# Kernel tuning notes

Hardware: AMD Instinct MI355X
Metric: run time of the kernel (lower is better)

Reference implementation:

```python
import jax, jax.numpy as jnp
import numpy as np

N_NODES = 50000
N_EDGES = 800000


def setup_inputs() -> dict:
    key = jax.random.key(0)
    ks = jax.random.split(key, 8)
    x = jax.random.normal(ks[0], (N_NODES, 128), dtype=jnp.float32)
    edge_index = jax.random.randint(ks[1], (2, N_EDGES), 0, N_NODES, dtype=jnp.int64)
    # GCNConv weights (PyG: x @ W then propagate, bias after aggregation)
    W1 = jax.random.normal(ks[2], (128, 256), dtype=jnp.float32) / np.sqrt(128)
    b1 = jnp.zeros((256,), dtype=jnp.float32)
    W2 = jax.random.normal(ks[3], (256, 128), dtype=jnp.float32) / np.sqrt(256)
    b2 = jnp.zeros((128,), dtype=jnp.float32)
    # projection head
    fcW1 = jax.random.normal(ks[4], (128, 128), dtype=jnp.float32) / np.sqrt(128)
    fcb1 = jnp.zeros((128,), dtype=jnp.float32)
    fcW2 = jax.random.normal(ks[5], (128, 128), dtype=jnp.float32) / np.sqrt(128)
    fcb2 = jnp.zeros((128,), dtype=jnp.float32)
    return {"x": x, "edge_index": edge_index, "W1": W1, "b1": b1,
            "W2": W2, "b2": b2, "fcW1": fcW1, "fcb1": fcb1,
            "fcW2": fcW2, "fcb2": fcb2}


def _gcn_conv(x, W, b, src, dst, dinv):
    # x' = D^-1/2 (A + I) D^-1/2 (x W) + b  (GCN with self-loops)
    xw = x @ W                                             # [N, C]
    coeff = dinv[src] * dinv[dst]                          # [E]
    msg = xw[src] * coeff[:, None]                         # [E, C] gather
    agg = jax.ops.segment_sum(msg, dst, num_segments=N_NODES)  # scatter-add
    self_term = xw * (dinv * dinv)[:, None]                # self-loop
    return agg + self_term + b


def reference(x, edge_index, W1, b1, W2, b2, fcW1, fcb1, fcW2, fcb2):
    src, dst = edge_index[0], edge_index[1]
    # degree of A + I (in-degree on dst, weight 1 each, +1 self-loop)
    deg = jax.ops.segment_sum(jnp.ones((N_EDGES,), jnp.float32), dst,
                              num_segments=N_NODES) + 1.0
    dinv = jax.lax.rsqrt(deg)
    # Encoder: GCNConv -> relu -> GCNConv -> relu
    h = jax.nn.relu(_gcn_conv(x, W1, b1, src, dst, dinv))
    z = jax.nn.relu(_gcn_conv(h, W2, b2, src, dst, dinv))
    # projection: Linear -> ELU -> Linear
    p = jax.nn.elu(z @ fcW1 + fcb1)
    return p @ fcW2 + fcb2
```

## Files before the change

### kernel.cpp

```cpp
#include <hip/hip_runtime.h>
#include <hip/hip_bf16.h>
#include <cstdint>

#define N_NODES 50000
#define N_EDGES 800000
#define C128 128
#define SCAN_BLOCKS ((N_NODES + 255) / 256)

typedef __attribute__((ext_vector_type(8))) short bf16x8;
typedef __attribute__((ext_vector_type(4))) float f32x4;
typedef unsigned int u32;

__device__ __forceinline__ bf16x8 pack_bf16x8(u32 a, u32 b, u32 c, u32 d) {
    union { u32 u[4]; bf16x8 v; } x;
    x.u[0] = a; x.u[1] = b; x.u[2] = c; x.u[3] = d;
    return x.v;
}

__device__ __forceinline__ bf16x8 as_bf16x8(uint4 v) {
    union { uint4 u; bf16x8 b; } x;
    x.u = v;
    return x.b;
}

__device__ __forceinline__ u32 rne_bf16(float x) {
    u32 u = __float_as_uint(x);
    return (u + 0x7FFFu + ((u >> 16) & 1u)) >> 16;
}

__device__ __forceinline__ void stage16(const u32* g, u32* lds) {
    __builtin_amdgcn_global_load_lds(
        (const __attribute__((address_space(1))) u32*)g,
        (__attribute__((address_space(3))) u32*)lds, 16, 0, 0);
}


__global__ void k_zero(int* __restrict__ a, int* __restrict__ b, int n) {
    int i = blockIdx.x * blockDim.x + threadIdx.x;
    if (i < n) { a[i] = 0; b[i] = 0; }
}

__device__ __forceinline__ int clamp_node(int v) {
    return v < 0 ? 0 : (v >= N_NODES ? N_NODES - 1 : v);
}

__global__ void k_count(const int* __restrict__ ei, int* __restrict__ counts) {
    int e = blockIdx.x * blockDim.x + threadIdx.x;
    if (e < N_EDGES) {
        int dst = clamp_node(ei[N_EDGES + e]);
        atomicAdd(&counts[dst], 1);
    }
}

__global__ void k_dinv(const int* __restrict__ counts, float* __restrict__ dinv) {
    int i = blockIdx.x * blockDim.x + threadIdx.x;
    if (i < N_NODES) {
        dinv[i] = rsqrtf((float)counts[i] + 1.0f);
    }
}

__global__ __launch_bounds__(256) void k_xscale(const float* __restrict__ x,
                                                const float* __restrict__ dinv,
                                                u32* __restrict__ xs ) {
    int idx = blockIdx.x * 256 + threadIdx.x;
    if (idx < N_NODES * 32) {
        int node = idx >> 5;
        float di = dinv[node];
        float4 v = reinterpret_cast<const float4*>(x)[idx];
        u32 w0 = rne_bf16(v.x * di) | (rne_bf16(v.y * di) << 16);
        u32 w1 = rne_bf16(v.z * di) | (rne_bf16(v.w * di) << 16);
        reinterpret_cast<uint2*>(xs)[idx] = make_uint2(w0, w1);
    }
}

__global__ __launch_bounds__(256) void k_scan1(const int* __restrict__ counts,
                                               int* __restrict__ part,
                                               int* __restrict__ bsum) {
    __shared__ int s[256];
    const int tid = threadIdx.x;
    const int i = blockIdx.x * 256 + tid;
    int v = (i < N_NODES) ? counts[i] : 0;
    s[tid] = v;
    __syncthreads();
    for (int off = 1; off < 256; off <<= 1) {
        int t = (tid >= off) ? s[tid - off] : 0;
        __syncthreads();
        s[tid] += t;
        __syncthreads();
    }
    if (i < N_NODES) part[i] = s[tid];
    if (tid == 255) bsum[blockIdx.x] = s[255];
}

__global__ __launch_bounds__(256) void k_scan2(const int* __restrict__ bsum,
                                               int* __restrict__ boff) {
    __shared__ int s[256];
    const int tid = threadIdx.x;
    int v = (tid < SCAN_BLOCKS) ? bsum[tid] : 0;
    s[tid] = v;
    __syncthreads();
    for (int off = 1; off < 256; off <<= 1) {
        int t = (tid >= off) ? s[tid - off] : 0;
        __syncthreads();
        s[tid] += t;
        __syncthreads();
    }
    if (tid < SCAN_BLOCKS) boff[tid] = s[tid] - v;
}

__global__ __launch_bounds__(256) void k_scan3(const int* __restrict__ part,
                                               const int* __restrict__ counts,
                                               const int* __restrict__ boff,
                                               int* __restrict__ offsets) {
    const int i = blockIdx.x * 256 + threadIdx.x;
    if (i < N_NODES) offsets[i] = part[i] - counts[i] + boff[blockIdx.x];
    if (i == 0) offsets[N_NODES] = N_EDGES;
}

__global__ void k_fill(const int* __restrict__ ei, const int* __restrict__ offsets,
                       int* __restrict__ cursor, int* __restrict__ csr) {
    int e = blockIdx.x * blockDim.x + threadIdx.x;
    if (e < N_EDGES) {
        int src = clamp_node(ei[e]);
        int dst = clamp_node(ei[N_EDGES + e]);
        int pos = atomicAdd(&cursor[dst], 1);
        int slot = offsets[dst] + pos;
        if (slot < N_EDGES) csr[slot] = src;
    }
}


__global__ __launch_bounds__(64) void k_prep(const float* __restrict__ W1,
                                             const float* __restrict__ W2,
                                             const float* __restrict__ fcW1,
                                             const float* __restrict__ fcW2,
                                             u32* __restrict__ ftab) {
    int bx = blockIdx.x;
    int s = bx >> 5, f = bx & 31;
    int kf = f >> 3, nf = f & 7;
    int l = threadIdx.x;
    const float* src; int ld, roff, coff;
    switch (s) {
        case 0:  src = W1;   ld = 256; roff = 0;   coff = 0;   break;
        case 1:  src = W1;   ld = 256; roff = 0;   coff = 128; break;
        case 2:  src = W2;   ld = 128; roff = 0;   coff = 0;   break;
        case 3:  src = W2;   ld = 128; roff = 128; coff = 0;   break;
        case 4:  src = fcW1; ld = 128; roff = 0;   coff = 0;   break;
        default: src = fcW2; ld = 128; roff = 0;   coff = 0;   break;
    }
    int col = coff + nf * 16 + (l & 15);
    int krow = roff + kf * 32 + (l >> 4) * 8;
    u32 hp[4], lp[4];
#pragma unroll
    for (int p = 0; p < 4; ++p) {
        float a0 = src[(size_t)(krow + 2 * p) * ld + col];
        float a1 = src[(size_t)(krow + 2 * p + 1) * ld + col];
        u32 h0 = __float_as_uint(a0) & 0xFFFF0000u;
        u32 h1 = __float_as_uint(a1) & 0xFFFF0000u;
        float r0 = a0 - __uint_as_float(h0);
        float r1 = a1 - __uint_as_float(h1);
        hp[p] = (h0 >> 16) | h1;
        lp[p] = ((__float_as_uint(r0) & 0xFFFF0000u) >> 16) |
                (__float_as_uint(r1) & 0xFFFF0000u);
    }
    u32* secb = ftab + (size_t)s * 16384;
    *reinterpret_cast<uint4*>(secb + (size_t)f * 256 + 4 * l)        = make_uint4(hp[0], hp[1], hp[2], hp[3]);
    *reinterpret_cast<uint4*>(secb + 8192 + (size_t)f * 256 + 4 * l) = make_uint4(lp[0], lp[1], lp[2], lp[3]);
}


template <bool HAS_BIAS, bool RELU>
__global__ __launch_bounds__(256) void k_prop(const u32* __restrict__ xs,
                                              float* __restrict__ out,
                                              const float* __restrict__ dinv,
                                              const int* __restrict__ offsets,
                                              const int* __restrict__ csr,
                                              const float* __restrict__ bias) {
    const int wave = threadIdx.x >> 6;
    const int lane = threadIdx.x & 63;
    const int half = lane >> 5;
    const int lc   = lane & 31;
    const int node = (blockIdx.x * 4 + wave) * 2 + half;
    if (node >= N_NODES) return;

    const uint2* __restrict__ xp = reinterpret_cast<const uint2*>(xs);
    const float di = dinv[node];

    uint2 sv = xp[(size_t)node * 32 + lc];
    float ax = __uint_as_float(sv.x << 16);
    float ay = __uint_as_float(sv.x & 0xFFFF0000u);
    float az = __uint_as_float(sv.y << 16);
    float aw = __uint_as_float(sv.y & 0xFFFF0000u);

    int e = offsets[node];
    const int eend = offsets[node + 1];
    for (; e + 4 <= eend; e += 4) {
        int s0 = csr[e + 0], s1 = csr[e + 1], s2 = csr[e + 2], s3 = csr[e + 3];
        uint2 v0 = xp[(size_t)s0 * 32 + lc];
        uint2 v1 = xp[(size_t)s1 * 32 + lc];
        uint2 v2 = xp[(size_t)s2 * 32 + lc];
        uint2 v3 = xp[(size_t)s3 * 32 + lc];
        ax += __uint_as_float(v0.x << 16);
        ay += __uint_as_float(v0.x & 0xFFFF0000u);
        az += __uint_as_float(v0.y << 16);
        aw += __uint_as_float(v0.y & 0xFFFF0000u);
        ax += __uint_as_float(v1.x << 16);
        ay += __uint_as_float(v1.x & 0xFFFF0000u);
        az += __uint_as_float(v1.y << 16);
        aw += __uint_as_float(v1.y & 0xFFFF0000u);
        ax += __uint_as_float(v2.x << 16);
        ay += __uint_as_float(v2.x & 0xFFFF0000u);
        az += __uint_as_float(v2.y << 16);
        aw += __uint_as_float(v2.y & 0xFFFF0000u);
        ax += __uint_as_float(v3.x << 16);
        ay += __uint_as_float(v3.x & 0xFFFF0000u);
        az += __uint_as_float(v3.y << 16);
        aw += __uint_as_float(v3.y & 0xFFFF0000u);
    }
    for (; e < eend; ++e) {
        int s = csr[e];
        uint2 v = xp[(size_t)s * 32 + lc];
        ax += __uint_as_float(v.x << 16);
        ay += __uint_as_float(v.x & 0xFFFF0000u);
        az += __uint_as_float(v.y << 16);
        aw += __uint_as_float(v.y & 0xFFFF0000u);
    }

    float4 o;
    o.x = di * ax; o.y = di * ay; o.z = di * az; o.w = di * aw;
    if (HAS_BIAS) {
        float4 bb = reinterpret_cast<const float4*>(bias)[lc];
        o.x += bb.x; o.y += bb.y; o.z += bb.z; o.w += bb.w;
    }
    if (RELU) {
        o.x = fmaxf(o.x, 0.0f); o.y = fmaxf(o.y, 0.0f);
        o.z = fmaxf(o.z, 0.0f); o.w = fmaxf(o.w, 0.0f);
    }
    reinterpret_cast<float4*>(out)[(size_t)node * 32 + lc] = o;
}


template <int NHALF, int ACT1, bool FINAL_BIAS, bool BF16_OUT>
__global__ __launch_bounds__(256, 3) void k_fused(
        const float* __restrict__ A,
        const u32* __restrict__ ftabW1,
        const u32* __restrict__ ftabW2,
        const float* __restrict__ b1v,
        const float* __restrict__ b2v,
        float* __restrict__ C,
        u32* __restrict__ C16,
        const float* __restrict__ dscale,
        int M) {
    __shared__ u32 lds_w[8192];

    const int tid = threadIdx.x;
    const int wave = tid >> 6, l = tid & 63;
    const int l15 = l & 15, l4 = l >> 4;
    const int r = blockIdx.x * 64 + wave * 16 + l15;
    const float* arow = A + (size_t)(r < M ? r : M - 1) * 128;

    auto stage_hi = [&](const u32* sec) {
#pragma unroll
        for (int i = 0; i < 8; ++i) {
            int off = i * 1024 + wave * 256;
            stage16(sec + off + 4 * l, lds_w + off);
        }
    };

    f32x4 accQ[8] = {};

    stage_hi(ftabW1);
    __syncthreads();

#pragma unroll
    for (int half = 0; half < NHALF; ++half) {
        const u32* w1lo = ftabW1 + (size_t)half * 16384 + 8192;
        const u32* w2lo = ftabW2 + (size_t)half * 16384 + 8192;

        f32x4 accH[8] = {};
#pragma unroll
        for (int kf = 0; kf < 4; ++kf) {
            uint4 wl[8];
#pragma unroll
            for (int nf = 0; nf < 8; ++nf)
                wl[nf] = *reinterpret_cast<const uint4*>(
                    w1lo + (size_t)(kf * 8 + nf) * 256 + 4 * l);

            const float* ap = arow + kf * 32 + l4 * 8;
            float4 v0 = *reinterpret_cast<const float4*>(ap);
            float4 v1 = *reinterpret_cast<const float4*>(ap + 4);
            float av[8] = {v0.x, v0.y, v0.z, v0.w, v1.x, v1.y, v1.z, v1.w};
            u32 hp[4], lp[4];
#pragma unroll
            for (int p = 0; p < 4; ++p) {
                float a0 = av[2 * p], a1 = av[2 * p + 1];
                u32 h0 = __float_as_uint(a0) & 0xFFFF0000u;
                u32 h1 = __float_as_uint(a1) & 0xFFFF0000u;
                float q0 = a0 - __uint_as_float(h0);
                float q1 = a1 - __uint_as_float(h1);
                hp[p] = (h0 >> 16) | h1;
                lp[p] = ((__float_as_uint(q0) & 0xFFFF0000u) >> 16) |
                        (__float_as_uint(q1) & 0xFFFF0000u);
            }
            bf16x8 ahi = pack_bf16x8(hp[0], hp[1], hp[2], hp[3]);
            bf16x8 alo = pack_bf16x8(lp[0], lp[1], lp[2], lp[3]);

#pragma unroll
            for (int nf = 0; nf < 8; ++nf) {
                bf16x8 whi = as_bf16x8(*reinterpret_cast<const uint4*>(
                    lds_w + (kf * 8 + nf) * 256 + 4 * l));
                bf16x8 wlo = as_bf16x8(wl[nf]);
                accH[nf] = __builtin_amdgcn_mfma_f32_16x16x32_bf16(whi, ahi, accH[nf], 0, 0, 0);
                accH[nf] = __builtin_amdgcn_mfma_f32_16x16x32_bf16(whi, alo, accH[nf], 0, 0, 0);
                accH[nf] = __builtin_amdgcn_mfma_f32_16x16x32_bf16(wlo, ahi, accH[nf], 0, 0, 0);
            }
        }
        __syncthreads();
        stage_hi(ftabW2 + (size_t)half * 16384);

        u32 hpk[8][4];
#pragma unroll
        for (int nf = 0; nf < 8; ++nf) {
            const float4 bb = *reinterpret_cast<const float4*>(
                b1v + half * 128 + nf * 16 + l4 * 4);
            const float bbv[4] = {bb.x, bb.y, bb.z, bb.w};
#pragma unroll
            for (int reg = 0; reg < 4; ++reg) {
                float v = accH[nf][reg] + bbv[reg];
                if (ACT1 == 1) v = fmaxf(v, 0.0f);
                else           v = v > 0.0f ? v : (expf(v) - 1.0f);
                u32 vh = __float_as_uint(v) & 0xFFFF0000u;
                float rr = v - __uint_as_float(vh);
                hpk[nf][reg] = (vh >> 16) | (__float_as_uint(rr) & 0xFFFF0000u);
            }
        }
        __syncthreads();

#pragma unroll
        for (int kf = 0; kf < 4; ++kf) {
            uint4 wl[8];
#pragma unroll
            for (int nf = 0; nf < 8; ++nf)
                wl[nf] = *reinterpret_cast<const uint4*>(
                    w2lo + (size_t)(kf * 8 + nf) * 256 + 4 * l);

            u32 got[8];
#pragma unroll
            for (int je = 0; je < 8; ++je) {
                int srcLane = ((l4 & 1) * 2 + (je >> 2)) * 16 + l15;
                u32 g0 = __shfl(hpk[2 * kf][je & 3], srcLane, 64);
                u32 g1 = __shfl(hpk[2 * kf + 1][je & 3], srcLane, 64);
                got[je] = (l4 & 2) ? g1 : g0;
            }
            u32 hh[4], gg[4];
#pragma unroll
            for (int p = 0; p < 4; ++p) {
                hh[p] = (got[2 * p] & 0xFFFFu) | (got[2 * p + 1] << 16);
                gg[p] = (got[2 * p] >> 16) | (got[2 * p + 1] & 0xFFFF0000u);
            }
            bf16x8 bh = pack_bf16x8(hh[0], hh[1], hh[2], hh[3]);
            bf16x8 bl = pack_bf16x8(gg[0], gg[1], gg[2], gg[3]);

#pragma unroll
            for (int nf = 0; nf < 8; ++nf) {
                bf16x8 whi = as_bf16x8(*reinterpret_cast<const uint4*>(
                    lds_w + (kf * 8 + nf) * 256 + 4 * l));
                bf16x8 wlo = as_bf16x8(wl[nf]);
                accQ[nf] = __builtin_amdgcn_mfma_f32_16x16x32_bf16(whi, bh, accQ[nf], 0, 0, 0);
                accQ[nf] = __builtin_amdgcn_mfma_f32_16x16x32_bf16(whi, bl, accQ[nf], 0, 0, 0);
                accQ[nf] = __builtin_amdgcn_mfma_f32_16x16x32_bf16(wlo, bh, accQ[nf], 0, 0, 0);
            }
        }

        if (half + 1 < NHALF) {
            __syncthreads();
            stage_hi(ftabW1 + (size_t)(half + 1) * 16384);
            __syncthreads();
        }
    }

    if (r < M) {
        if (BF16_OUT) {
            float sc = dscale[r];
#pragma unroll
            for (int nf = 0; nf < 8; ++nf) {
                u32 w0 = rne_bf16(accQ[nf][0] * sc) | (rne_bf16(accQ[nf][1] * sc) << 16);
                u32 w1 = rne_bf16(accQ[nf][2] * sc) | (rne_bf16(accQ[nf][3] * sc) << 16);
                reinterpret_cast<uint2*>(C16)[(size_t)r * 32 + nf * 4 + l4] =
                    make_uint2(w0, w1);
            }
        } else {
#pragma unroll
            for (int nf = 0; nf < 8; ++nf) {
                float4 v;
                v.x = accQ[nf][0]; v.y = accQ[nf][1];
                v.z = accQ[nf][2]; v.w = accQ[nf][3];
                if (FINAL_BIAS) {
                    const float4 bb = *reinterpret_cast<const float4*>(b2v + nf * 16 + l4 * 4);
                    v.x += bb.x; v.y += bb.y; v.z += bb.z; v.w += bb.w;
                }
                *reinterpret_cast<float4*>(C + (size_t)r * 128 + nf * 16 + l4 * 4) = v;
            }
        }
    }
}


extern "C" void kernel_launch(void* const* d_in, const int* in_sizes, int n_in,
                              void* d_out, int out_size, void* d_ws, size_t ws_size,
                              hipStream_t stream) {
    const float* x    = (const float*)d_in[0];
    const int*   ei   = (const int*)d_in[1];
    const float* W1   = (const float*)d_in[2];
    const float* b1   = (const float*)d_in[3];
    const float* W2   = (const float*)d_in[4];
    const float* b2   = (const float*)d_in[5];
    const float* fcW1 = (const float*)d_in[6];
    const float* fcb1 = (const float*)d_in[7];
    const float* fcW2 = (const float*)d_in[8];
    const float* fcb2 = (const float*)d_in[9];
    float* out        = (float*)d_out;

    char* ws = (char*)d_ws;
    size_t off = 0;
    auto alloc = [&](size_t bytes) {
        void* p = ws + off;
        off += (bytes + 255) & ~(size_t)255;
        return p;
    };
    int*   counts  = (int*)alloc(N_NODES * sizeof(int));
    int*   cursor  = (int*)alloc(N_NODES * sizeof(int));
    int*   part    = (int*)alloc(N_NODES * sizeof(int));
    int*   bsum    = (int*)alloc(SCAN_BLOCKS * sizeof(int));
    int*   boff    = (int*)alloc(SCAN_BLOCKS * sizeof(int));
    int*   offsets = (int*)alloc((N_NODES + 1) * sizeof(int));
    int*   csr     = (int*)alloc(N_EDGES * sizeof(int));
    float* dinv    = (float*)alloc(N_NODES * sizeof(float));
    u32*   ftab    = (u32*)alloc((size_t)6 * 16384 * sizeof(u32));
    u32*   xs      = (u32*)alloc((size_t)N_NODES * 128 * 2);
    u32*   qs      = (u32*)alloc((size_t)N_NODES * 128 * 2);
    (void)ws_size; (void)n_in; (void)in_sizes; (void)out_size;

    const u32 SEC = 16384;

    k_zero<<<(N_NODES + 255) / 256, 256, 0, stream>>>(counts, cursor, N_NODES);
    k_prep<<<192, 64, 0, stream>>>(W1, W2, fcW1, fcW2, ftab);
    k_count<<<(N_EDGES + 255) / 256, 256, 0, stream>>>(ei, counts);
    k_dinv<<<(N_NODES + 255) / 256, 256, 0, stream>>>(counts, dinv);
    k_xscale<<<(N_NODES * 32 + 255) / 256, 256, 0, stream>>>(x, dinv, xs);
    k_scan1<<<SCAN_BLOCKS, 256, 0, stream>>>(counts, part, bsum);
    k_scan2<<<1, 256, 0, stream>>>(bsum, boff);
    k_scan3<<<SCAN_BLOCKS, 256, 0, stream>>>(part, counts, boff, offsets);
    k_fill<<<(N_EDGES + 255) / 256, 256, 0, stream>>>(ei, offsets, cursor, csr);

    const int prop_grid = (N_NODES + 7) / 8;
    const int gm = (N_NODES + 63) / 64;

    k_prop<false, false><<<prop_grid, 256, 0, stream>>>(xs, out, dinv, offsets, csr, nullptr);

    k_fused<2, 1, false, true><<<gm, 256, 0, stream>>>(out, ftab, ftab + 2 * SEC,
                                                       b1, nullptr, nullptr, qs, dinv, N_NODES);

    k_prop<true, true><<<prop_grid, 256, 0, stream>>>(qs, out, dinv, offsets, csr, b2);

    k_fused<1, 2, true, false><<<gm, 256, 0, stream>>>(out, ftab + 4 * SEC, ftab + 5 * SEC,
                                                       fcb1, fcb2, out, nullptr, nullptr, N_NODES);
}
```

Before: 238.6 us.

## Stage both hi and lo weight fragments in LDS and hoist A-row split

The weight fragment table is reorganised so each fragment's hi and lo bf16 halves sit next to each other (512-word stride). The fused MLP kernel now stages the whole section, hi and lo, into a doubled 64KB LDS buffer instead of reading the lo half from global memory per k-step. The input row's bf16 hi/lo split is also hoisted out of the half loop and computed once. In exchange the LDS use doubles and the occupancy hint drops from 3 to 2 blocks per CU, and the hoisted A fragments hold more registers.

```diff
diff --git a/kernel.cpp b/kernel.cpp
--- a/kernel.cpp
+++ b/kernel.cpp
@@ -163,9 +163,9 @@
         lp[p] = ((__float_as_uint(r0) & 0xFFFF0000u) >> 16) |
                 (__float_as_uint(r1) & 0xFFFF0000u);
     }
-    u32* secb = ftab + (size_t)s * 16384;
-    *reinterpret_cast<uint4*>(secb + (size_t)f * 256 + 4 * l)        = make_uint4(hp[0], hp[1], hp[2], hp[3]);
-    *reinterpret_cast<uint4*>(secb + 8192 + (size_t)f * 256 + 4 * l) = make_uint4(lp[0], lp[1], lp[2], lp[3]);
+    u32* dst = ftab + (size_t)s * 16384 + (size_t)f * 512;
+    *reinterpret_cast<uint4*>(dst + 4 * l)       = make_uint4(hp[0], hp[1], hp[2], hp[3]);
+    *reinterpret_cast<uint4*>(dst + 256 + 4 * l) = make_uint4(lp[0], lp[1], lp[2], lp[3]);
 }
 
 
@@ -241,7 +241,7 @@
 
 
 template <int NHALF, int ACT1, bool FINAL_BIAS, bool BF16_OUT>
-__global__ __launch_bounds__(256, 3) void k_fused(
+__global__ __launch_bounds__(256, 2) void k_fused(
         const float* __restrict__ A,
         const u32* __restrict__ ftabW1,
         const u32* __restrict__ ftabW2,
@@ -251,7 +251,7 @@
         u32* __restrict__ C16,
         const float* __restrict__ dscale,
         int M) {
-    __shared__ u32 lds_w[8192];
+    __shared__ u32 lds_w[16384];
 
     const int tid = threadIdx.x;
     const int wave = tid >> 6, l = tid & 63;
@@ -259,64 +259,58 @@
     const int r = blockIdx.x * 64 + wave * 16 + l15;
     const float* arow = A + (size_t)(r < M ? r : M - 1) * 128;
 
-    auto stage_hi = [&](const u32* sec) {
-#pragma unroll
-        for (int i = 0; i < 8; ++i) {
-            int off = i * 1024 + wave * 256;
+    auto stage_sec = [&](const u32* sec) {
+#pragma unroll
+        for (int i = 0; i < 16; ++i) {
+            int off = (i * 4 + wave) * 256;
             stage16(sec + off + 4 * l, lds_w + off);
         }
     };
 
+    bf16x8 ahi[4], alo[4];
+#pragma unroll
+    for (int kf = 0; kf < 4; ++kf) {
+        const float* ap = arow + kf * 32 + l4 * 8;
+        float4 v0 = *reinterpret_cast<const float4*>(ap);
+        float4 v1 = *reinterpret_cast<const float4*>(ap + 4);
+        float av[8] = {v0.x, v0.y, v0.z, v0.w, v1.x, v1.y, v1.z, v1.w};
+        u32 hp[4], lp[4];
+#pragma unroll
+        for (int p = 0; p < 4; ++p) {
+            float a0 = av[2 * p], a1 = av[2 * p + 1];
+            u32 h0 = __float_as_uint(a0) & 0xFFFF0000u;
+            u32 h1 = __float_as_uint(a1) & 0xFFFF0000u;
+            float q0 = a0 - __uint_as_float(h0);
+            float q1 = a1 - __uint_as_float(h1);
+            hp[p] = (h0 >> 16) | h1;
+            lp[p] = ((__float_as_uint(q0) & 0xFFFF0000u) >> 16) |
+                    (__float_as_uint(q1) & 0xFFFF0000u);
+        }
+        ahi[kf] = pack_bf16x8(hp[0], hp[1], hp[2], hp[3]);
+        alo[kf] = pack_bf16x8(lp[0], lp[1], lp[2], lp[3]);
+    }
+
     f32x4 accQ[8] = {};
 
-    stage_hi(ftabW1);
+    stage_sec(ftabW1);
     __syncthreads();
 
-#pragma unroll
     for (int half = 0; half < NHALF; ++half) {
-        const u32* w1lo = ftabW1 + (size_t)half * 16384 + 8192;
-        const u32* w2lo = ftabW2 + (size_t)half * 16384 + 8192;
-
         f32x4 accH[8] = {};
 #pragma unroll
         for (int kf = 0; kf < 4; ++kf) {
-            uint4 wl[8];
-#pragma unroll
-            for (int nf = 0; nf < 8; ++nf)
-                wl[nf] = *reinterpret_cast<const uint4*>(
-                    w1lo + (size_t)(kf * 8 + nf) * 256 + 4 * l);
-
-            const float* ap = arow + kf * 32 + l4 * 8;
-            float4 v0 = *reinterpret_cast<const float4*>(ap);
-            float4 v1 = *reinterpret_cast<const float4*>(ap + 4);
-            float av[8] = {v0.x, v0.y, v0.z, v0.w, v1.x, v1.y, v1.z, v1.w};
-            u32 hp[4], lp[4];
-#pragma unroll
-            for (int p = 0; p < 4; ++p) {
-                float a0 = av[2 * p], a1 = av[2 * p + 1];
-                u32 h0 = __float_as_uint(a0) & 0xFFFF0000u;
-                u32 h1 = __float_as_uint(a1) & 0xFFFF0000u;
-                float q0 = a0 - __uint_as_float(h0);
-                float q1 = a1 - __uint_as_float(h1);
-                hp[p] = (h0 >> 16) | h1;
-                lp[p] = ((__float_as_uint(q0) & 0xFFFF0000u) >> 16) |
-                        (__float_as_uint(q1) & 0xFFFF0000u);
-            }
-            bf16x8 ahi = pack_bf16x8(hp[0], hp[1], hp[2], hp[3]);
-            bf16x8 alo = pack_bf16x8(lp[0], lp[1], lp[2], lp[3]);
-
 #pragma unroll
             for (int nf = 0; nf < 8; ++nf) {
-                bf16x8 whi = as_bf16x8(*reinterpret_cast<const uint4*>(
-                    lds_w + (kf * 8 + nf) * 256 + 4 * l));
-                bf16x8 wlo = as_bf16x8(wl[nf]);
-                accH[nf] = __builtin_amdgcn_mfma_f32_16x16x32_bf16(whi, ahi, accH[nf], 0, 0, 0);
-                accH[nf] = __builtin_amdgcn_mfma_f32_16x16x32_bf16(whi, alo, accH[nf], 0, 0, 0);
-                accH[nf] = __builtin_amdgcn_mfma_f32_16x16x32_bf16(wlo, ahi, accH[nf], 0, 0, 0);
-            }
-        }
-        __syncthreads();
-        stage_hi(ftabW2 + (size_t)half * 16384);
+                const u32* fb = lds_w + (kf * 8 + nf) * 512;
+                bf16x8 whi = as_bf16x8(*reinterpret_cast<const uint4*>(fb + 4 * l));
+                bf16x8 wlo = as_bf16x8(*reinterpret_cast<const uint4*>(fb + 256 + 4 * l));
+                accH[nf] = __builtin_amdgcn_mfma_f32_16x16x32_bf16(whi, ahi[kf], accH[nf], 0, 0, 0);
+                accH[nf] = __builtin_amdgcn_mfma_f32_16x16x32_bf16(whi, alo[kf], accH[nf], 0, 0, 0);
+                accH[nf] = __builtin_amdgcn_mfma_f32_16x16x32_bf16(wlo, ahi[kf], accH[nf], 0, 0, 0);
+            }
+        }
+        __syncthreads();
+        stage_sec(ftabW2 + (size_t)half * 16384);
 
         u32 hpk[8][4];
 #pragma unroll
@@ -338,12 +332,6 @@
 
 #pragma unroll
         for (int kf = 0; kf < 4; ++kf) {
-            uint4 wl[8];
-#pragma unroll
-            for (int nf = 0; nf < 8; ++nf)
-                wl[nf] = *reinterpret_cast<const uint4*>(
-                    w2lo + (size_t)(kf * 8 + nf) * 256 + 4 * l);
-
             u32 got[8];
 #pragma unroll
             for (int je = 0; je < 8; ++je) {
@@ -363,9 +351,9 @@
 
 #pragma unroll
             for (int nf = 0; nf < 8; ++nf) {
-                bf16x8 whi = as_bf16x8(*reinterpret_cast<const uint4*>(
-                    lds_w + (kf * 8 + nf) * 256 + 4 * l));
-                bf16x8 wlo = as_bf16x8(wl[nf]);
+                const u32* fb = lds_w + (kf * 8 + nf) * 512;
+                bf16x8 whi = as_bf16x8(*reinterpret_cast<const uint4*>(fb + 4 * l));
+                bf16x8 wlo = as_bf16x8(*reinterpret_cast<const uint4*>(fb + 256 + 4 * l));
                 accQ[nf] = __builtin_amdgcn_mfma_f32_16x16x32_bf16(whi, bh, accQ[nf], 0, 0, 0);
                 accQ[nf] = __builtin_amdgcn_mfma_f32_16x16x32_bf16(whi, bl, accQ[nf], 0, 0, 0);
                 accQ[nf] = __builtin_amdgcn_mfma_f32_16x16x32_bf16(wlo, bh, accQ[nf], 0, 0, 0);
@@ -374,7 +362,7 @@
 
         if (half + 1 < NHALF) {
             __syncthreads();
-            stage_hi(ftabW1 + (size_t)(half + 1) * 16384);
+            stage_sec(ftabW1 + (size_t)(half + 1) * 16384);
             __syncthreads();
         }
     }
```

After: 237.5 us. Within noise of the previous version (-0.5%).
